# Kernel optimization log

Hardware: AMD Instinct MI355X
Metric: run time of the kernel (lower is better)

The kernel has to match this reference:

```python
import jax, jax.numpy as jnp
import numpy as np

SQRT3 = 3.0 ** 0.5
MAX_RADIUS = 5.0
NUM_BASIS = 10
NUM_NEIGHBORS = 15.0
# e3nn soft_one_hot_linspace 'smooth_finite' prefactor: 1.14136 * e^2
SMOOTH_C = 1.14136 * float(np.exp(2.0))


def _sus(x):
    # smooth compactly-supported bump helper: exp(-1/x) for x>0 else 0
    return jnp.where(x > 0.0, jnp.exp(-1.0 / jnp.where(x > 0.0, x, 1.0)), 0.0)


def _soft_one_hot(x):
    # e3nn soft_one_hot_linspace(start=0, end=5, number=10, basis='smooth_finite', cutoff=True)
    values = jnp.linspace(0.0, MAX_RADIUS, NUM_BASIS + 2)[1:-1]  # interior knots
    step = MAX_RADIUS / (NUM_BASIS + 1)
    diff = (x[:, None] - values) / step  # [E, 10]
    return SMOOTH_C * _sus(diff + 1.0) * _sus(1.0 - diff)


def _sh_l1(v, normalize):
    # spherical harmonics up to lmax=1, 'component' normalization.
    # e3nn l=1 component ordering is (y, z, x), each scaled by sqrt(3).
    if normalize:
        v = v / (jnp.linalg.norm(v, axis=-1, keepdims=True) + 1e-9)
    x, y, z = v[..., 0], v[..., 1], v[..., 2]
    return jnp.stack([jnp.ones_like(x), SQRT3 * y, SQRT3 * z, SQRT3 * x], axis=-1)


def setup_inputs() -> dict:
    key = jax.random.key(0)
    ks = jax.random.split(key, 12)
    N, E, G, Fin, D, L, A, H = 100000, 800000, 64, 16, 32, 3, 4, 64
    pos = jax.random.normal(ks[0], (N, 3), jnp.float32) * 1.5
    x = jax.random.normal(ks[1], (N, Fin), jnp.float32)
    orientation = jax.random.uniform(ks[2], (G, 2), jnp.float32)
    edge_src = jax.random.randint(ks[3], (E,), 0, N)
    edge_dst = jax.random.randint(ks[4], (E,), 0, N)
    batch = jnp.sort(jax.random.randint(ks[5], (N,), 0, G))
    W_embed = jax.random.normal(ks[6], (Fin, D), jnp.float32)
    W_tp = jax.random.normal(ks[7], (L, D, A, D), jnp.float32)
    W_fc1 = jax.random.normal(ks[8], (L, NUM_BASIS, H), jnp.float32)
    W_fc2 = jax.random.normal(ks[9], (L, H, 1), jnp.float32)
    W_dec = jax.random.normal(ks[10], (D, A), jnp.float32)
    return {"pos": pos, "x": x, "orientation": orientation, "W_embed": W_embed,
            "W_tp": W_tp, "W_fc1": W_fc1, "W_fc2": W_fc2, "W_dec": W_dec,
            "edge_src": edge_src, "edge_dst": edge_dst, "batch": batch}


def reference(pos, x, orientation, W_embed, W_tp, W_fc1, W_fc2, W_dec,
              edge_src, edge_dst, batch):
    N = x.shape[0]
    G = orientation.shape[0]
    D = W_embed.shape[1]
    A = W_tp.shape[2]
    H = W_fc1.shape[2]

    edge_vec = pos[edge_src] - pos[edge_dst]            # [E, 3]
    edge_len = jnp.linalg.norm(edge_vec, axis=-1)       # [E]
    edge_attr = _sh_l1(edge_vec, True)                  # [E, 4]
    edge_len_emb = _soft_one_hot(edge_len) * (NUM_BASIS ** 0.5)  # [E, 10]

    h = x @ W_embed  # embedding o3.Linear -> [N, D]
    tp_norm = 1.0 / float(np.sqrt(D * A))
    fc1_norm = 1.0 / float(np.sqrt(NUM_BASIS))
    fc2_norm = 1.0 / float(np.sqrt(H))
    agg_norm = 1.0 / float(np.sqrt(NUM_NEIGHBORS))

    for l in range(W_tp.shape[0]):  # fixed small layer count
        h_src = h[edge_src]  # gather [E, D]
        # fully-connected tensor product (bilinear): contract node features with
        # weights first to keep the big intermediate at [E, A, D]
        t = jnp.einsum('ei,iak->eak', h_src, W_tp[l])
        ang = jnp.einsum('eak,ea->ek', t, edge_attr) * tp_norm  # [E, D]
        hid = jax.nn.silu(edge_len_emb @ W_fc1[l] * fc1_norm)   # [E, 64]
        rad = hid @ W_fc2[l] * fc2_norm                          # [E, 1]
        msg = ang * rad                                          # [E, D]
        agg = jax.ops.segment_sum(msg, edge_dst, num_segments=N)
        h = h + agg * agg_norm  # residual

    # graph mean pooling
    gsum = jax.ops.segment_sum(h, batch, num_segments=G)
    cnt = jax.ops.segment_sum(jnp.ones((N,), jnp.float32), batch, num_segments=G)
    graph = gsum / jnp.maximum(cnt, 1.0)[:, None]  # [G, D]

    sh_coeffs = graph @ W_dec  # decoder o3.Linear -> [G, 4]
    theta, phi = orientation[..., 0], orientation[..., 1]
    q = jnp.stack([jnp.sin(theta) * jnp.cos(phi),
                   jnp.sin(theta) * jnp.sin(phi),
                   jnp.cos(theta)], axis=-1)  # unit vectors [G, 3]
    sh_q = _sh_l1(q, False)
    return (sh_coeffs * sh_q).sum(axis=-1)  # [G]
```

## Files before the change

kernel.cpp:

```cpp
#include <hip/hip_runtime.h>


constexpr int Dk  = 32;
constexpr int Hk  = 64;
constexpr int NBk = 10;
constexpr int Lk  = 3;
constexpr int FinK = 16;
constexpr int TAB = 8192;
constexpr int SCB = 256;

__device__ __forceinline__ float sus(float x) {
    return x > 0.f ? __expf(-1.f / x) : 0.f;
}

__device__ __forceinline__ unsigned pack_bf16_rne(float a, float b) {
    unsigned ua = __float_as_uint(a), ub = __float_as_uint(b);
    ua += 0x7FFFu + ((ua >> 16) & 1u);
    ub += 0x7FFFu + ((ub >> 16) & 1u);
    return (ua >> 16) | (ub & 0xFFFF0000u);
}

__global__ __launch_bounds__(256) void radial_tab_k(
    const float* __restrict__ Wfc1, const float* __restrict__ Wfc2,
    float* __restrict__ rtab)
{
    int l = blockIdx.y;
    __shared__ float sW1[NBk * Hk];
    __shared__ float sW2[Hk];
    for (int j = threadIdx.x; j < NBk * Hk; j += blockDim.x) sW1[j] = Wfc1[l * NBk * Hk + j];
    for (int j = threadIdx.x; j < Hk; j += blockDim.x) sW2[j] = Wfc2[l * Hk + j];
    __syncthreads();

    int i = blockIdx.x * blockDim.x + threadIdx.x;
    if (i > TAB) return;
    float len = 5.f * (float)i / (float)TAB;
    const float C_EMB = (float)(1.14136 * 7.3890560989306495);
    float t = len * 2.2f;
    float emb[NBk];
#pragma unroll
    for (int j = 0; j < NBk; j++) {
        float d1 = t - (float)j;
        float d2 = (float)(j + 2) - t;
        emb[j] = C_EMB * sus(d1) * sus(d2);
    }
    const float C_OUT = (float)(0.125 * 0.08838834764831845 * 0.2581988897471611);
    float r = 0.f;
    for (int j = 0; j < Hk; j++) {
        float a = 0.f;
#pragma unroll
        for (int b = 0; b < NBk; b++) a += emb[b] * sW1[b * Hk + j];
        float sg = 1.f / (1.f + __expf(-a));
        r += a * sg * sW2[j];
    }
    rtab[l * (TAB + 1) + i] = r * C_OUT;
}

__global__ __launch_bounds__(256) void hist_k(
    const int* __restrict__ edst, int* __restrict__ deg, int E)
{
    int e = blockIdx.x * blockDim.x + threadIdx.x;
    if (e < E) atomicAdd(&deg[edst[e]], 1);
}

__global__ __launch_bounds__(SCB) void scan1_k(
    const int* __restrict__ deg, int* __restrict__ incl,
    int* __restrict__ bsum, int N)
{
    __shared__ int s[SCB];
    int g = blockIdx.x * SCB + threadIdx.x;
    s[threadIdx.x] = (g < N) ? deg[g] : 0;
    __syncthreads();
    for (int off = 1; off < SCB; off <<= 1) {
        int t = (threadIdx.x >= off) ? s[threadIdx.x - off] : 0;
        __syncthreads();
        s[threadIdx.x] += t;
        __syncthreads();
    }
    if (g < N) incl[g] = s[threadIdx.x];
    if (threadIdx.x == SCB - 1) bsum[blockIdx.x] = s[threadIdx.x];
}

__global__ __launch_bounds__(512) void scan2_k(int* __restrict__ bsum, int nb)
{
    __shared__ int s[512];
    s[threadIdx.x] = (threadIdx.x < nb) ? bsum[threadIdx.x] : 0;
    __syncthreads();
    for (int off = 1; off < 512; off <<= 1) {
        int t = (threadIdx.x >= off) ? s[threadIdx.x - off] : 0;
        __syncthreads();
        s[threadIdx.x] += t;
        __syncthreads();
    }
    if (threadIdx.x < nb) bsum[threadIdx.x] = s[threadIdx.x];
}

__global__ __launch_bounds__(SCB) void scan3_k(
    const int* __restrict__ deg, const int* __restrict__ incl,
    const int* __restrict__ bsum, int* __restrict__ row_ptr,
    int* __restrict__ cur, int N, int E)
{
    int g = blockIdx.x * SCB + threadIdx.x;
    if (g < N) {
        int off = (blockIdx.x > 0) ? bsum[blockIdx.x - 1] : 0;
        int excl = incl[g] - deg[g] + off;
        row_ptr[g] = excl;
        cur[g] = excl;
    }
    if (g == 0) row_ptr[N] = E;
}

__global__ __launch_bounds__(256) void place_k(
    const int* __restrict__ edst, int* __restrict__ cur,
    int* __restrict__ perm, int E)
{
    int e = blockIdx.x * blockDim.x + threadIdx.x;
    if (e >= E) return;
    int p = atomicAdd(&cur[edst[e]], 1);
    perm[p] = e;
}

__global__ __launch_bounds__(256) void fill_k(
    const int* __restrict__ perm, const int* __restrict__ esrc,
    const int* __restrict__ edst, const float* __restrict__ pos,
    const float* __restrict__ rtab,
    int* __restrict__ esrc2, float* __restrict__ aY,
    float* __restrict__ aZ, float* __restrict__ aX,
    float* __restrict__ cfac2, int E)
{
    int p = blockIdx.x * blockDim.x + threadIdx.x;
    if (p >= E) return;
    int e = perm[p];
    int s = esrc[e], d = edst[e];
    float vx = pos[3 * s + 0] - pos[3 * d + 0];
    float vy = pos[3 * s + 1] - pos[3 * d + 1];
    float vz = pos[3 * s + 2] - pos[3 * d + 2];
    float len = sqrtf(vx * vx + vy * vy + vz * vz);
    float inv = 1.f / (len + 1e-9f);
    const float S3 = 1.7320508075688772f;

    float xx = fminf(len * ((float)TAB / 5.f), (float)TAB);
    int i = min((int)xx, TAB - 1);
    float f = xx - (float)i;

    esrc2[p] = s;
    aY[p] = S3 * vy * inv;
    aZ[p] = S3 * vz * inv;
    aX[p] = S3 * vx * inv;
#pragma unroll
    for (int l = 0; l < Lk; l++) {
        float a = rtab[l * (TAB + 1) + i];
        float b = rtab[l * (TAB + 1) + i + 1];
        cfac2[(size_t)l * E + p] = a + (b - a) * f;
    }
}

__global__ __launch_bounds__(256) void embed_k(
    const float* __restrict__ x, const float* __restrict__ We,
    float* __restrict__ h, int N)
{
    __shared__ float sW[FinK * Dk];
    for (int i = threadIdx.x; i < FinK * Dk; i += blockDim.x) sW[i] = We[i];
    __syncthreads();
    int tid = blockIdx.x * blockDim.x + threadIdx.x;
    int n = tid >> 5, k = tid & 31;
    if (n >= N) return;
    float acc = 0.f;
#pragma unroll
    for (int i = 0; i < FinK; i++) acc += x[n * FinK + i] * sW[i * Dk + k];
    h[n * Dk + k] = acc;
}

__global__ __launch_bounds__(256) void tp_gemm(
    const float* __restrict__ h, const float* __restrict__ Wl,
    unsigned* __restrict__ HpU, int N)
{
    int tid = blockIdx.x * blockDim.x + threadIdx.x;
    int n = tid >> 5, k = tid & 31;
    if (n >= N) return;
    float hv = h[(size_t)n * Dk + k];
    float a0 = 0.f, a1 = 0.f, a2 = 0.f, a3 = 0.f;
#pragma unroll
    for (int i = 0; i < Dk; i++) {
        float hb = __shfl(hv, i, 32);
        a0 += hb * Wl[i * 128 + 0 * 32 + k];
        a1 += hb * Wl[i * 128 + 1 * 32 + k];
        a2 += hb * Wl[i * 128 + 2 * 32 + k];
        a3 += hb * Wl[i * 128 + 3 * 32 + k];
    }
    unsigned* o = HpU + (size_t)n * 64;
    o[2 * k]     = pack_bf16_rne(a0, a1);
    o[2 * k + 1] = pack_bf16_rne(a2, a3);
}

__global__ __launch_bounds__(256) void agg_k(
    const unsigned* __restrict__ HpU, const float* __restrict__ aY,
    const float* __restrict__ aZ, const float* __restrict__ aX,
    const float* __restrict__ cl, const int* __restrict__ esrc2,
    const int* __restrict__ row_ptr, float* __restrict__ h, int N)
{
    int tid = blockIdx.x * blockDim.x + threadIdx.x;
    int n = tid >> 5, k = tid & 31;
    if (n >= N) return;
    int r0 = row_ptr[n], r1 = row_ptr[n + 1];
    float acc = 0.f;
    for (int i = r0; i < r1; ++i) {
        int s = esrc2[i];
        float ay = aY[i], az = aZ[i], ax = aX[i];
        float c = cl[i];
        uint2 u = ((const uint2*)(HpU + (size_t)s * 64))[k];
        float h0 = __uint_as_float(u.x << 16);
        float h1 = __uint_as_float(u.x & 0xFFFF0000u);
        float h2 = __uint_as_float(u.y << 16);
        float h3 = __uint_as_float(u.y & 0xFFFF0000u);
        acc += c * (h0 + ay * h1 + az * h2 + ax * h3);
    }
    h[(size_t)n * Dk + k] += acc;
}

constexpr int POOL_NPB = 512;
__global__ __launch_bounds__(256) void pool_k(
    const float* __restrict__ h, const int* __restrict__ batch,
    float* __restrict__ gsum, float* __restrict__ cnt, int N)
{
    int k = threadIdx.x & 31;
    int row = threadIdx.x >> 5;
    int start = blockIdx.x * POOL_NPB;
    int end = min(start + POOL_NPB, N);
    int curg = -1;
    float acc = 0.f, cacc = 0.f;
    for (int n = start + row; n < end; n += 8) {
        int g = batch[n];
        float v = h[(size_t)n * Dk + k];
        if (g != curg) {
            if (curg >= 0) {
                unsafeAtomicAdd(&gsum[curg * Dk + k], acc);
                if (k == 0) unsafeAtomicAdd(&cnt[curg], cacc);
            }
            curg = g; acc = 0.f; cacc = 0.f;
        }
        acc += v; cacc += 1.f;
    }
    if (curg >= 0) {
        unsafeAtomicAdd(&gsum[curg * Dk + k], acc);
        if (k == 0) unsafeAtomicAdd(&cnt[curg], cacc);
    }
}

__global__ __launch_bounds__(64) void final_k(
    const float* __restrict__ gsum, const float* __restrict__ cnt,
    const float* __restrict__ Wdec, const float* __restrict__ orient,
    float* __restrict__ out, int G)
{
    int g = blockIdx.x * blockDim.x + threadIdx.x;
    if (g >= G) return;
    float ic = 1.f / fmaxf(cnt[g], 1.f);
    float c0 = 0.f, c1 = 0.f, c2 = 0.f, c3 = 0.f;
#pragma unroll
    for (int i = 0; i < Dk; i++) {
        float gv = gsum[g * Dk + i] * ic;
        c0 += gv * Wdec[i * 4 + 0];
        c1 += gv * Wdec[i * 4 + 1];
        c2 += gv * Wdec[i * 4 + 2];
        c3 += gv * Wdec[i * 4 + 3];
    }
    float th = orient[g * 2 + 0], ph = orient[g * 2 + 1];
    float st = sinf(th), ct = cosf(th), sp = sinf(ph), cp = cosf(ph);
    float qx = st * cp, qy = st * sp, qz = ct;
    const float S3 = 1.7320508075688772f;
    out[g] = c0 + c1 * S3 * qy + c2 * S3 * qz + c3 * S3 * qx;
}

extern "C" void kernel_launch(void* const* d_in, const int* in_sizes, int n_in,
                              void* d_out, int out_size, void* d_ws, size_t ws_size,
                              hipStream_t stream) {
    const float* pos     = (const float*)d_in[0];
    const float* x       = (const float*)d_in[1];
    const float* orient  = (const float*)d_in[2];
    const float* W_embed = (const float*)d_in[3];
    const float* W_tp    = (const float*)d_in[4];
    const float* W_fc1   = (const float*)d_in[5];
    const float* W_fc2   = (const float*)d_in[6];
    const float* W_dec   = (const float*)d_in[7];
    const int*   esrc    = (const int*)d_in[8];
    const int*   edst    = (const int*)d_in[9];
    const int*   batch   = (const int*)d_in[10];

    const int N = in_sizes[0] / 3;
    const int E = in_sizes[8];
    const int G = in_sizes[2] / 2;
    const int NB = (N + SCB - 1) / SCB;

    float*    ws     = (float*)d_ws;
    float*    cfac2  = ws;
    float*    aY     = cfac2 + (size_t)3 * E;
    float*    aZ     = aY + E;
    float*    aX     = aZ + E;
    float*    h      = aX + E;
    unsigned* HpU    = (unsigned*)(h + (size_t)Dk * N);
    float*    gsum   = (float*)(HpU + (size_t)64 * N);
    float*    cnt    = gsum + (size_t)Dk * G;
    float*    rtab   = cnt + G;
    int*      esrc2  = (int*)(rtab + 3 * (TAB + 1));
    int*      perm   = esrc2 + E;
    int*      deg    = perm + E;
    int*      incl   = deg + N;
    int*      row_ptr= incl + N;
    int*      cur    = row_ptr + (N + 1);
    int*      bsum   = cur + N;

    hipMemsetAsync(deg, 0, (size_t)N * sizeof(int), stream);
    hipMemsetAsync(gsum, 0, (size_t)(Dk * G + G) * sizeof(float), stream);

    {
        dim3 grid((TAB + 1 + 255) / 256, Lk);
        radial_tab_k<<<grid, 256, 0, stream>>>(W_fc1, W_fc2, rtab);
    }
    hist_k<<<(E + 255) / 256, 256, 0, stream>>>(edst, deg, E);
    scan1_k<<<NB, SCB, 0, stream>>>(deg, incl, bsum, N);
    scan2_k<<<1, 512, 0, stream>>>(bsum, NB);
    scan3_k<<<NB, SCB, 0, stream>>>(deg, incl, bsum, row_ptr, cur, N, E);

    place_k<<<(E + 255) / 256, 256, 0, stream>>>(edst, cur, perm, E);
    fill_k<<<(E + 255) / 256, 256, 0, stream>>>(
        perm, esrc, edst, pos, rtab, esrc2, aY, aZ, aX, cfac2, E);
    embed_k<<<(N * 32 + 255) / 256, 256, 0, stream>>>(x, W_embed, h, N);

    for (int l = 0; l < Lk; l++) {
        tp_gemm<<<(N * 32 + 255) / 256, 256, 0, stream>>>(
            h, W_tp + (size_t)l * Dk * 4 * Dk, HpU, N);
        agg_k<<<(N * 32 + 255) / 256, 256, 0, stream>>>(
            HpU, aY, aZ, aX, cfac2 + (size_t)l * E, esrc2, row_ptr, h, N);
    }

    pool_k<<<(N + POOL_NPB - 1) / POOL_NPB, 256, 0, stream>>>(h, batch, gsum, cnt, N);
    final_k<<<(G + 63) / 64, 64, 0, stream>>>(gsum, cnt, W_dec, orient, (float*)d_out, G);
}
```

Before: 587.7 us.

## Aggregate raw bf16 node features before applying the tensor-product weights

Reorders the per-layer computation so each node first gathers its neighbours' bf16 features (32 values instead of 128), weighted by precomputed per-edge coefficient×attribute float4s. The W_tp contraction then runs once per destination node after aggregation, which fuses tp_gemm into the aggregation kernel. The goal is to cut gather traffic per edge and one kernel launch per layer. In exchange, per-edge attribute storage grows to a float4 per layer, and the bf16 rounding now applies to h before the GEMM rather than to its output, which changes numerics slightly.

Result: faster. 503.8 us (-14.3%).

```diff
diff --git a/kernel.cpp b/kernel.cpp
--- a/kernel.cpp
+++ b/kernel.cpp
@@ -123,9 +123,7 @@
     const int* __restrict__ perm, const int* __restrict__ esrc,
     const int* __restrict__ edst, const float* __restrict__ pos,
     const float* __restrict__ rtab,
-    int* __restrict__ esrc2, float* __restrict__ aY,
-    float* __restrict__ aZ, float* __restrict__ aX,
-    float* __restrict__ cfac2, int E)
+    int* __restrict__ esrc2, float4* __restrict__ cattr4, int E)
 {
     int p = blockIdx.x * blockDim.x + threadIdx.x;
     if (p >= E) return;
@@ -137,26 +135,25 @@
     float len = sqrtf(vx * vx + vy * vy + vz * vz);
     float inv = 1.f / (len + 1e-9f);
     const float S3 = 1.7320508075688772f;
+    float ay = S3 * vy * inv, az = S3 * vz * inv, ax = S3 * vx * inv;
 
     float xx = fminf(len * ((float)TAB / 5.f), (float)TAB);
     int i = min((int)xx, TAB - 1);
     float f = xx - (float)i;
 
     esrc2[p] = s;
-    aY[p] = S3 * vy * inv;
-    aZ[p] = S3 * vz * inv;
-    aX[p] = S3 * vx * inv;
 #pragma unroll
     for (int l = 0; l < Lk; l++) {
         float a = rtab[l * (TAB + 1) + i];
         float b = rtab[l * (TAB + 1) + i + 1];
-        cfac2[(size_t)l * E + p] = a + (b - a) * f;
+        float c = a + (b - a) * f;
+        cattr4[(size_t)l * E + p] = make_float4(c, c * ay, c * az, c * ax);
     }
 }
 
 __global__ __launch_bounds__(256) void embed_k(
     const float* __restrict__ x, const float* __restrict__ We,
-    float* __restrict__ h, int N)
+    float* __restrict__ h, unsigned* __restrict__ hb, int N)
 {
     __shared__ float sW[FinK * Dk];
     for (int i = threadIdx.x; i < FinK * Dk; i += blockDim.x) sW[i] = We[i];
@@ -167,54 +164,50 @@
     float acc = 0.f;
 #pragma unroll
     for (int i = 0; i < FinK; i++) acc += x[n * FinK + i] * sW[i * Dk + k];
-    h[n * Dk + k] = acc;
-}
-
-__global__ __launch_bounds__(256) void tp_gemm(
-    const float* __restrict__ h, const float* __restrict__ Wl,
-    unsigned* __restrict__ HpU, int N)
-{
-    int tid = blockIdx.x * blockDim.x + threadIdx.x;
-    int n = tid >> 5, k = tid & 31;
-    if (n >= N) return;
-    float hv = h[(size_t)n * Dk + k];
-    float a0 = 0.f, a1 = 0.f, a2 = 0.f, a3 = 0.f;
-#pragma unroll
-    for (int i = 0; i < Dk; i++) {
-        float hb = __shfl(hv, i, 32);
-        a0 += hb * Wl[i * 128 + 0 * 32 + k];
-        a1 += hb * Wl[i * 128 + 1 * 32 + k];
-        a2 += hb * Wl[i * 128 + 2 * 32 + k];
-        a3 += hb * Wl[i * 128 + 3 * 32 + k];
-    }
-    unsigned* o = HpU + (size_t)n * 64;
-    o[2 * k]     = pack_bf16_rne(a0, a1);
-    o[2 * k + 1] = pack_bf16_rne(a2, a3);
-}
-
-__global__ __launch_bounds__(256) void agg_k(
-    const unsigned* __restrict__ HpU, const float* __restrict__ aY,
-    const float* __restrict__ aZ, const float* __restrict__ aX,
-    const float* __restrict__ cl, const int* __restrict__ esrc2,
-    const int* __restrict__ row_ptr, float* __restrict__ h, int N)
+    h[(size_t)n * Dk + k] = acc;
+    float partner = __shfl(acc, k | 1, 32);
+    if ((k & 1) == 0) hb[(size_t)n * 16 + (k >> 1)] = pack_bf16_rne(acc, partner);
+}
+
+__global__ __launch_bounds__(256) void agg_tp_k(
+    const unsigned* __restrict__ hb_in,
+    const float4* __restrict__ cattr4,
+    const int* __restrict__ esrc2, const int* __restrict__ row_ptr,
+    const float* __restrict__ Wl,
+    float* __restrict__ h,
+    unsigned* __restrict__ hb_out,
+    int N)
 {
     int tid = blockIdx.x * blockDim.x + threadIdx.x;
     int n = tid >> 5, k = tid & 31;
     if (n >= N) return;
     int r0 = row_ptr[n], r1 = row_ptr[n + 1];
-    float acc = 0.f;
+
+    float a0 = 0.f, a1 = 0.f, a2 = 0.f, a3 = 0.f;
     for (int i = r0; i < r1; ++i) {
         int s = esrc2[i];
-        float ay = aY[i], az = aZ[i], ax = aX[i];
-        float c = cl[i];
-        uint2 u = ((const uint2*)(HpU + (size_t)s * 64))[k];
-        float h0 = __uint_as_float(u.x << 16);
-        float h1 = __uint_as_float(u.x & 0xFFFF0000u);
-        float h2 = __uint_as_float(u.y << 16);
-        float h3 = __uint_as_float(u.y & 0xFFFF0000u);
-        acc += c * (h0 + ay * h1 + az * h2 + ax * h3);
-    }
-    h[(size_t)n * Dk + k] += acc;
+        float4 ca = cattr4[i];
+        unsigned u = hb_in[(size_t)s * 16 + (k >> 1)];
+        float hk = (k & 1) ? __uint_as_float(u & 0xFFFF0000u)
+                           : __uint_as_float(u << 16);
+        a0 += ca.x * hk; a1 += ca.y * hk; a2 += ca.z * hk; a3 += ca.w * hk;
+    }
+
+    float out = 0.f;
+#pragma unroll
+    for (int i = 0; i < Dk; i++) {
+        float b0 = __shfl(a0, i, 32);
+        float b1 = __shfl(a1, i, 32);
+        float b2 = __shfl(a2, i, 32);
+        float b3 = __shfl(a3, i, 32);
+        const float* w = Wl + i * 128 + k;
+        out += b0 * w[0] + b1 * w[32] + b2 * w[64] + b3 * w[96];
+    }
+
+    float hn = h[(size_t)n * Dk + k] + out;
+    h[(size_t)n * Dk + k] = hn;
+    float partner = __shfl(hn, k | 1, 32);
+    if ((k & 1) == 0) hb_out[(size_t)n * 16 + (k >> 1)] = pack_bf16_rne(hn, partner);
 }
 
 constexpr int POOL_NPB = 512;
@@ -291,13 +284,11 @@
     const int NB = (N + SCB - 1) / SCB;
 
     float*    ws     = (float*)d_ws;
-    float*    cfac2  = ws;
-    float*    aY     = cfac2 + (size_t)3 * E;
-    float*    aZ     = aY + E;
-    float*    aX     = aZ + E;
-    float*    h      = aX + E;
-    unsigned* HpU    = (unsigned*)(h + (size_t)Dk * N);
-    float*    gsum   = (float*)(HpU + (size_t)64 * N);
+    float4*   cattr4 = (float4*)ws;
+    float*    h      = ws + (size_t)12 * E;
+    unsigned* hb0    = (unsigned*)(h + (size_t)Dk * N);
+    unsigned* hb1    = hb0 + (size_t)16 * N;
+    float*    gsum   = (float*)(hb1 + (size_t)16 * N);
     float*    cnt    = gsum + (size_t)Dk * G;
     float*    rtab   = cnt + G;
     int*      esrc2  = (int*)(rtab + 3 * (TAB + 1));
@@ -322,14 +313,14 @@
 
     place_k<<<(E + 255) / 256, 256, 0, stream>>>(edst, cur, perm, E);
     fill_k<<<(E + 255) / 256, 256, 0, stream>>>(
-        perm, esrc, edst, pos, rtab, esrc2, aY, aZ, aX, cfac2, E);
-    embed_k<<<(N * 32 + 255) / 256, 256, 0, stream>>>(x, W_embed, h, N);
-
+        perm, esrc, edst, pos, rtab, esrc2, cattr4, E);
+    embed_k<<<(N * 32 + 255) / 256, 256, 0, stream>>>(x, W_embed, h, hb0, N);
+
+    unsigned* hbuf[2] = {hb0, hb1};
     for (int l = 0; l < Lk; l++) {
-        tp_gemm<<<(N * 32 + 255) / 256, 256, 0, stream>>>(
-            h, W_tp + (size_t)l * Dk * 4 * Dk, HpU, N);
-        agg_k<<<(N * 32 + 255) / 256, 256, 0, stream>>>(
-            HpU, aY, aZ, aX, cfac2 + (size_t)l * E, esrc2, row_ptr, h, N);
+        agg_tp_k<<<(N * 32 + 255) / 256, 256, 0, stream>>>(
+            hbuf[l & 1], cattr4 + (size_t)l * E, esrc2, row_ptr,
+            W_tp + (size_t)l * Dk * 4 * Dk, h, hbuf[(l + 1) & 1], N);
     }
 
     pool_k<<<(N + POOL_NPB - 1) / POOL_NPB, 256, 0, stream>>>(h, batch, gsum, cnt, N);
```
